# Optimization experiments

Hardware: AMD Instinct MI355X
Metric: run time of the kernel (lower is better)

## Reference

```python
import jax, jax.numpy as jnp
import numpy as np

N_NODES = 100000
N_EDGES = 1600000
IN_DIM, HID, OUT_DIM = 64, 128, 9


def _lin_params(key, fan_in, fan_out, bias=True):
    k1, k2 = jax.random.split(key)
    bound = 1.0 / np.sqrt(fan_in)
    W = jax.random.uniform(k1, (fan_in, fan_out), jnp.float32, -bound, bound)
    if bias:
        b = jax.random.uniform(k2, (fan_out,), jnp.float32, -bound, bound)
        return W, b
    return W


def setup_inputs() -> dict:
    key = jax.random.key(0)
    ks = jax.random.split(key, 12)
    x = jax.random.normal(ks[0], (N_NODES, IN_DIM), jnp.float32)
    edge_index = jax.random.randint(ks[1], (2, N_EDGES), 0, N_NODES, jnp.int64 if jax.config.jax_enable_x64 else jnp.int32)
    Wl1, bl1 = _lin_params(ks[2], IN_DIM, HID)
    Wr1 = _lin_params(ks[3], IN_DIM, HID, bias=False)
    Wl2, bl2 = _lin_params(ks[4], HID, HID)
    Wr2 = _lin_params(ks[5], HID, HID, bias=False)
    Wl3, bl3 = _lin_params(ks[6], HID, 2 * HID)
    Wr3 = _lin_params(ks[7], HID, 2 * HID, bias=False)
    Wfc, bfc = _lin_params(ks[8], 2 * HID, OUT_DIM)
    return {"x": x, "edge_index": edge_index,
            "Wl1": Wl1, "bl1": bl1, "Wr1": Wr1,
            "Wl2": Wl2, "bl2": bl2, "Wr2": Wr2,
            "Wl3": Wl3, "bl3": bl3, "Wr3": Wr3,
            "Wfc": Wfc, "bfc": bfc}


def _sage_conv(x, src, dst, Wl, bl, Wr):
    # PyG SAGEConv (mean aggr): out = lin_l(mean_{j->i} x_j) + lin_r(x_i)
    n = x.shape[0]
    summed = jax.ops.segment_sum(x[src], dst, num_segments=n)         # [N, d]
    deg = jax.ops.segment_sum(jnp.ones((src.shape[0],), x.dtype), dst, num_segments=n)
    mean = summed / jnp.maximum(deg, 1.0)[:, None]
    return mean @ Wl + bl + x @ Wr


def reference(x, edge_index, Wl1, bl1, Wr1, Wl2, bl2, Wr2, Wl3, bl3, Wr3, Wfc, bfc):
    src, dst = edge_index[0], edge_index[1]
    h = jax.nn.relu(_sage_conv(x, src, dst, Wl1, bl1, Wr1))
    h = jax.nn.relu(_sage_conv(h, src, dst, Wl2, bl2, Wr2))
    h = jax.nn.relu(_sage_conv(h, src, dst, Wl3, bl3, Wr3))
    return h @ Wfc + bfc
```

## Files before the change

kernel.cpp:

```cpp
#include <hip/hip_runtime.h>
#include <cstddef>
#include <cstdint>


typedef unsigned int uint_t;
typedef unsigned short ushort_t;
typedef __attribute__((ext_vector_type(8))) short short8;
typedef __attribute__((ext_vector_type(4))) float f32x4;

#define N_IN 64
#define N_HID 128
#define N_OUT 9
#define EB 512
#define NBUCK_MAX 800

__device__ __forceinline__ ushort_t f2bf(float f) {
    uint_t u = __float_as_uint(f);
    u += 0x7fffu + ((u >> 16) & 1u);
    return (ushort_t)(u >> 16);
}
__device__ __forceinline__ float bf2f(ushort_t h) {
    return __uint_as_float(((uint_t)h) << 16);
}
__device__ __forceinline__ void async_ld16(const void* g, void* l) {
    __builtin_amdgcn_global_load_lds((const __attribute__((address_space(1))) void*)g,
                                     (__attribute__((address_space(3))) void*)l, 16, 0, 0);
}

__global__ __launch_bounds__(256) void csr_count(const int* __restrict__ dst,
                                                 uint_t* __restrict__ cnt,
                                                 int E, int nbuck, int chunk) {
    __shared__ uint_t c[NBUCK_MAX];
    for (int i = threadIdx.x; i < nbuck; i += 256) c[i] = 0;
    __syncthreads();
    const int beg = blockIdx.x * chunk;
    const int end = min(beg + chunk, E);
    for (int i = beg + threadIdx.x; i < end; i += 256)
        atomicAdd(&c[dst[i] >> 7], 1u);
    __syncthreads();
    for (int i = threadIdx.x; i < nbuck; i += 256)
        cnt[(size_t)blockIdx.x * nbuck + i] = c[i];
}

__global__ __launch_bounds__(512) void csr_colscan(uint_t* __restrict__ cnt,
                                                   uint_t* __restrict__ total, int nbuck) {
    __shared__ uint_t sm[512];
    const int b = blockIdx.x;
    const uint_t v = cnt[(size_t)threadIdx.x * nbuck + b];
    sm[threadIdx.x] = v;
    __syncthreads();
    for (int off = 1; off < 512; off <<= 1) {
        uint_t t = (threadIdx.x >= off) ? sm[threadIdx.x - off] : 0;
        __syncthreads();
        sm[threadIdx.x] += t;
        __syncthreads();
    }
    cnt[(size_t)threadIdx.x * nbuck + b] = sm[threadIdx.x] - v;
    if (threadIdx.x == 511) total[b] = sm[511];
}

__global__ __launch_bounds__(1024) void top_scan_1024(const uint_t* __restrict__ total,
                                                      uint_t* __restrict__ basev, int nb) {
    __shared__ uint_t sm[1024];
    const int i = threadIdx.x;
    const uint_t v = (i < nb) ? total[i] : 0;
    sm[i] = v;
    __syncthreads();
    for (int off = 1; off < 1024; off <<= 1) {
        uint_t t = (i >= off) ? sm[i - off] : 0;
        __syncthreads();
        sm[i] += t;
        __syncthreads();
    }
    if (i < nb) basev[i] = sm[i] - v;
}

__global__ __launch_bounds__(256) void csr_scatter(const int* __restrict__ src,
                                                   const int* __restrict__ dst,
                                                   const uint_t* __restrict__ cnt,
                                                   const uint_t* __restrict__ basev,
                                                   uint_t* __restrict__ ebuf,
                                                   int E, int nbuck, int chunk) {
    __shared__ uint_t cur[NBUCK_MAX];
    for (int i = threadIdx.x; i < nbuck; i += 256)
        cur[i] = basev[i] + cnt[(size_t)blockIdx.x * nbuck + i];
    __syncthreads();
    const int beg = blockIdx.x * chunk;
    const int end = min(beg + chunk, E);
    for (int i = beg + threadIdx.x; i < end; i += 256) {
        const int d = dst[i];
        const uint_t pos = atomicAdd(&cur[d >> 7], 1u);
        ebuf[pos] = ((uint_t)src[i] << 7) | (uint_t)(d & 127);
    }
}

__global__ __launch_bounds__(256) void csr_final(const uint_t* __restrict__ ebuf,
                                                 const uint_t* __restrict__ basev,
                                                 const uint_t* __restrict__ total,
                                                 int* __restrict__ colA,
                                                 int* __restrict__ row_start,
                                                 int* __restrict__ degi,
                                                 float* __restrict__ invdeg, int M) {
    __shared__ uint_t c128[128];
    __shared__ uint_t cur[128];
    __shared__ uint_t sm[256];
    const int b = blockIdx.x;
    const int nbase = b << 7;
    const uint_t e0 = basev[b];
    const uint_t T = total[b];
    if (threadIdx.x < 128) c128[threadIdx.x] = 0;
    __syncthreads();
    for (uint_t i = threadIdx.x; i < T; i += 256)
        atomicAdd(&c128[ebuf[e0 + i] & 127], 1u);
    __syncthreads();
    const uint_t v = (threadIdx.x < 128) ? c128[threadIdx.x] : 0;
    sm[threadIdx.x] = v;
    __syncthreads();
    for (int off = 1; off < 128; off <<= 1) {
        uint_t t = (threadIdx.x >= off) ? sm[threadIdx.x - off] : 0;
        __syncthreads();
        sm[threadIdx.x] += t;
        __syncthreads();
    }
    if (threadIdx.x < 128) {
        const uint_t ex = sm[threadIdx.x] - v;
        cur[threadIdx.x] = ex;
        const int node = nbase + threadIdx.x;
        if (node < M) {
            degi[node] = (int)v;
            invdeg[node] = 1.0f / fmaxf((float)v, 1.0f);
            row_start[node] = (int)(e0 + ex);
        }
    }
    __syncthreads();
    for (uint_t i = threadIdx.x; i < T; i += 256) {
        const uint_t p = ebuf[e0 + i];
        const uint_t pos = atomicAdd(&cur[p & 127], 1u);
        colA[e0 + pos] = (int)(p >> 7);
    }
}

__global__ void split_x_kernel(const float* __restrict__ X, ushort_t* __restrict__ xh,
                               ushort_t* __restrict__ xl, ushort_t* __restrict__ xrow, int M) {
    int idx = blockIdx.x * 256 + threadIdx.x;
    if (idx >= M * 8) return;
    const int node = idx >> 3;
    const int ch = idx & 7;
    const float4 f0 = *(const float4*)(X + (size_t)node * 64 + ch * 8);
    const float4 f1 = *(const float4*)(X + (size_t)node * 64 + ch * 8 + 4);
    float e[8] = {f0.x, f0.y, f0.z, f0.w, f1.x, f1.y, f1.z, f1.w};
    uint_t hv[4], lv[4];
#pragma unroll
    for (int t = 0; t < 4; ++t) {
        ushort_t h0 = f2bf(e[2 * t]), h1 = f2bf(e[2 * t + 1]);
        ushort_t l0 = f2bf(e[2 * t] - bf2f(h0)), l1 = f2bf(e[2 * t + 1] - bf2f(h1));
        hv[t] = (uint_t)h0 | ((uint_t)h1 << 16);
        lv[t] = (uint_t)l0 | ((uint_t)l1 << 16);
    }
    const size_t off = ((size_t)(node >> 7) * 8 + ch) * 1024 + (node & 127) * 8;
    const uint4 hq = make_uint4(hv[0], hv[1], hv[2], hv[3]);
    *(uint4*)(xh + off) = hq;
    *(uint4*)(xl + off) = make_uint4(lv[0], lv[1], lv[2], lv[3]);
    *(uint4*)(xrow + (size_t)node * 64 + ch * 8) = hq;
}

__global__ __launch_bounds__(256) void wsplit_all(
    const float* __restrict__ Wl1, const float* __restrict__ Wr1,
    const float* __restrict__ Wl2, const float* __restrict__ Wr2,
    const float* __restrict__ Wl3, const float* __restrict__ Wr3,
    ushort_t* __restrict__ w1lh, ushort_t* __restrict__ w1ll,
    ushort_t* __restrict__ w1rh, ushort_t* __restrict__ w1rl,
    ushort_t* __restrict__ w2lh, ushort_t* __restrict__ w2ll,
    ushort_t* __restrict__ w2rh, ushort_t* __restrict__ w2rl,
    ushort_t* __restrict__ w3lh, ushort_t* __restrict__ w3ll,
    ushort_t* __restrict__ w3rh, ushort_t* __restrict__ w3rl)
{
    int idx = blockIdx.x * 256 + threadIdx.x;
    const float* W; ushort_t* th; ushort_t* tl; int K, N, e;
    if (idx < 8192)        { W = Wl1; th = w1lh; tl = w1ll; K = 64;  N = 128; e = idx; }
    else if (idx < 16384)  { W = Wr1; th = w1rh; tl = w1rl; K = 64;  N = 128; e = idx - 8192; }
    else if (idx < 32768)  { W = Wl2; th = w2lh; tl = w2ll; K = 128; N = 128; e = idx - 16384; }
    else if (idx < 49152)  { W = Wr2; th = w2rh; tl = w2rl; K = 128; N = 128; e = idx - 32768; }
    else if (idx < 81920)  { W = Wl3; th = w3lh; tl = w3ll; K = 128; N = 256; e = idx - 49152; }
    else if (idx < 114688) { W = Wr3; th = w3rh; tl = w3rl; K = 128; N = 256; e = idx - 81920; }
    else return;
    int k = e / N, n = e - k * N;
    float v = W[e];
    ushort_t hb = f2bf(v);
    const size_t off = ((size_t)(n >> 7) * (K >> 3) + (k >> 3)) * 1024 + (n & 127) * 8 + (k & 7);
    th[off] = hb;
    tl[off] = f2bf(v - bf2f(hb));
}

__device__ __forceinline__ void acc8_hi(float* a, uint4 h) {
    a[0] += __uint_as_float(h.x << 16);
    a[1] += __uint_as_float(h.x & 0xffff0000u);
    a[2] += __uint_as_float(h.y << 16);
    a[3] += __uint_as_float(h.y & 0xffff0000u);
    a[4] += __uint_as_float(h.z << 16);
    a[5] += __uint_as_float(h.z & 0xffff0000u);
    a[6] += __uint_as_float(h.w << 16);
    a[7] += __uint_as_float(h.w & 0xffff0000u);
}

template <int CH>
__global__ __launch_bounds__(256) void gather_mean_hi(
    const ushort_t* __restrict__ fh, const int* __restrict__ colA,
    const int* __restrict__ row_start, const int* __restrict__ degi,
    const float* __restrict__ invdeg,
    ushort_t* __restrict__ oh, int M)
{
    constexpr int SLOTS = 256 / CH;
    constexpr int DIM = CH * 8;
    const int tid = threadIdx.x;
    const int slot = tid / CH;
    const int ch = tid % CH;
    const int node = blockIdx.x * SLOTS + slot;
    if (node >= M) return;
    const int beg = row_start[node];
    const int cnt = degi[node];
    float a[8];
#pragma unroll
    for (int t = 0; t < 8; ++t) a[t] = 0.f;
    int j = 0;
    for (; j + 3 < cnt; j += 4) {
        const int s0 = colA[beg + j];
        const int s1 = colA[beg + j + 1];
        const int s2 = colA[beg + j + 2];
        const int s3 = colA[beg + j + 3];
        const uint4 h0 = *(const uint4*)(fh + (size_t)s0 * DIM + ch * 8);
        const uint4 h1 = *(const uint4*)(fh + (size_t)s1 * DIM + ch * 8);
        const uint4 h2 = *(const uint4*)(fh + (size_t)s2 * DIM + ch * 8);
        const uint4 h3 = *(const uint4*)(fh + (size_t)s3 * DIM + ch * 8);
        acc8_hi(a, h0);
        acc8_hi(a, h1);
        acc8_hi(a, h2);
        acc8_hi(a, h3);
    }
    for (; j < cnt; ++j) {
        const int s0 = colA[beg + j];
        const uint4 h0 = *(const uint4*)(fh + (size_t)s0 * DIM + ch * 8);
        acc8_hi(a, h0);
    }
    const float sc = invdeg[node];
    uint_t hv[4];
#pragma unroll
    for (int t = 0; t < 4; ++t) {
        ushort_t hb0 = f2bf(a[2 * t] * sc), hb1 = f2bf(a[2 * t + 1] * sc);
        hv[t] = (uint_t)hb0 | ((uint_t)hb1 << 16);
    }
    const size_t off = ((size_t)(node >> 7) * CH + ch) * 1024 + (node & 127) * 8;
    *(uint4*)(oh + off) = make_uint4(hv[0], hv[1], hv[2], hv[3]);
}

__global__ __launch_bounds__(256) void mfma_sage_gemm(
    const ushort_t* __restrict__ Amh,
    const ushort_t* __restrict__ Axh, const ushort_t* __restrict__ Axl,
    const ushort_t* __restrict__ Blh, const ushort_t* __restrict__ Bll,
    const ushort_t* __restrict__ Brh, const ushort_t* __restrict__ Brl,
    const float* __restrict__ bias, ushort_t* __restrict__ Oh,
    ushort_t* __restrict__ Orow,
    int M, int K, int N, int axl_valid)
{
    __shared__ ushort_t As_h[4096];
    __shared__ ushort_t As_l[4096];
    __shared__ ushort_t Bs_h[4096];
    __shared__ ushort_t Bs_l[4096];

    const int tid  = threadIdx.x;
    const int lane = tid & 63;
    const int wave = tid >> 6;
    const int wm = (wave & 1) * 64;
    const int wn = (wave >> 1) * 64;
    const int l15 = lane & 15;
    const int quad = lane >> 4;
    const int bm = blockIdx.x * 128;
    const int bn = blockIdx.y * 128;
    const int KC = K >> 3;

    const int s0 = wave * 1024 + lane * 8;
    const int s1 = s0 + 512;
    const size_t gA_w = ((size_t)blockIdx.x * KC + wave) << 10;
    const size_t gB_w = ((size_t)blockIdx.y * KC + wave) << 10;
    const int l8 = lane * 8;

    f32x4 acc[4][4];
#pragma unroll
    for (int i = 0; i < 4; ++i)
#pragma unroll
        for (int j = 0; j < 4; ++j) acc[i][j] = (f32x4){0.f, 0.f, 0.f, 0.f};

    for (int phase = 0; phase < 2; ++phase) {
        const ushort_t* __restrict__ Ah = phase ? Axh : Amh;
        const ushort_t* __restrict__ Al = phase ? Axl : (const ushort_t*)nullptr;
        const ushort_t* __restrict__ Bh = phase ? Brh : Blh;
        const ushort_t* __restrict__ Bl = phase ? Brl : Bll;
        const bool doAl = (phase == 1) && (axl_valid != 0);
        for (int k0 = 0; k0 < K; k0 += 32) {
            const size_t ga = gA_w + ((size_t)(k0 >> 3) << 10) + l8;
            const size_t gb = gB_w + ((size_t)(k0 >> 3) << 10) + l8;
            __syncthreads();
            async_ld16(Ah + ga, &As_h[s0]);
            async_ld16(Ah + ga + 512, &As_h[s1]);
            if (doAl) {
                async_ld16(Al + ga, &As_l[s0]);
                async_ld16(Al + ga + 512, &As_l[s1]);
            }
            async_ld16(Bh + gb, &Bs_h[s0]);
            async_ld16(Bh + gb + 512, &Bs_h[s1]);
            async_ld16(Bl + gb, &Bs_l[s0]);
            async_ld16(Bl + gb + 512, &Bs_l[s1]);
            __syncthreads();

            short8 fah[4], fal[4], fbh[4], fbl[4];
#pragma unroll
            for (int i = 0; i < 4; ++i) {
                const int aoff = quad * 1024 + (wm + i * 16 + l15) * 8;
                const int boff = quad * 1024 + (wn + i * 16 + l15) * 8;
                fah[i] = *(const short8*)&As_h[aoff];
                fbh[i] = *(const short8*)&Bs_h[boff];
                fbl[i] = *(const short8*)&Bs_l[boff];
                if (doAl) fal[i] = *(const short8*)&As_l[aoff];
            }
#pragma unroll
            for (int i = 0; i < 4; ++i)
#pragma unroll
                for (int j = 0; j < 4; ++j) {
                    acc[i][j] = __builtin_amdgcn_mfma_f32_16x16x32_bf16(fah[i], fbh[j], acc[i][j], 0, 0, 0);
                    acc[i][j] = __builtin_amdgcn_mfma_f32_16x16x32_bf16(fah[i], fbl[j], acc[i][j], 0, 0, 0);
                    if (doAl)
                        acc[i][j] = __builtin_amdgcn_mfma_f32_16x16x32_bf16(fal[i], fbh[j], acc[i][j], 0, 0, 0);
                }
        }
    }

    const size_t otile = (size_t)blockIdx.x * (N >> 3) * 1024;
#pragma unroll
    for (int i = 0; i < 4; ++i) {
        const int mr0 = wm + i * 16 + quad * 4;
#pragma unroll
        for (int j = 0; j < 4; ++j) {
            const int col = bn + wn + j * 16 + l15;
            const float bv = bias[col];
            const size_t cbase = otile + (size_t)(col >> 3) * 1024 + (col & 7);
#pragma unroll
            for (int r = 0; r < 4; ++r) {
                const int row = bm + mr0 + r;
                if (row < M) {
                    float y = fmaxf(acc[i][j][r] + bv, 0.f);
                    const ushort_t hb = f2bf(y);
                    Oh[cbase + (size_t)(mr0 + r) * 8] = hb;
                    if (Orow) Orow[(size_t)row * N + col] = hb;
                }
            }
        }
    }
}

__global__ __launch_bounds__(256) void fc_hi_kernel(
    const ushort_t* __restrict__ hh, const float* __restrict__ W,
    const float* __restrict__ b, float* __restrict__ outp, int M)
{
    __shared__ float Ws[256 * N_OUT];
    __shared__ float bs[N_OUT];
    for (int i = threadIdx.x; i < 256 * N_OUT; i += 256) Ws[i] = W[i];
    if (threadIdx.x < N_OUT) bs[threadIdx.x] = b[threadIdx.x];
    __syncthreads();
    const int t = blockIdx.x * 256 + threadIdx.x;
    if (t >= M * N_OUT) return;
    const int i = t / N_OUT;
    const int j = t - i * N_OUT;
    const ushort_t* __restrict__ base = hh + (size_t)(i >> 7) * 32 * 1024 + (i & 127) * 8;
    float s = bs[j];
#pragma unroll 4
    for (int c = 0; c < 32; ++c) {
        const uint4 v = *(const uint4*)(base + (size_t)c * 1024);
        const uint_t u[4] = {v.x, v.y, v.z, v.w};
#pragma unroll
        for (int q = 0; q < 4; ++q) {
            float a0 = __uint_as_float(u[q] << 16);
            float a1 = __uint_as_float(u[q] & 0xffff0000u);
            s += a0 * Ws[(c * 8 + 2 * q) * N_OUT + j] + a1 * Ws[(c * 8 + 2 * q + 1) * N_OUT + j];
        }
    }
    outp[t] = s;
}

extern "C" void kernel_launch(void* const* d_in, const int* in_sizes, int n_in,
                              void* d_out, int out_size, void* d_ws, size_t ws_size,
                              hipStream_t stream) {
    const float* x   = (const float*)d_in[0];
    const int*   ei  = (const int*)d_in[1];
    const float* Wl1 = (const float*)d_in[2];
    const float* bl1 = (const float*)d_in[3];
    const float* Wr1 = (const float*)d_in[4];
    const float* Wl2 = (const float*)d_in[5];
    const float* bl2 = (const float*)d_in[6];
    const float* Wr2 = (const float*)d_in[7];
    const float* Wl3 = (const float*)d_in[8];
    const float* bl3 = (const float*)d_in[9];
    const float* Wr3 = (const float*)d_in[10];
    const float* Wfc = (const float*)d_in[11];
    const float* bfc = (const float*)d_in[12];
    float* outp = (float*)d_out;

    const int M = in_sizes[0] / N_IN;
    const int E = in_sizes[1] / 2;
    const int* src = ei;
    const int* dst = ei + E;
    const size_t Mrow = 100352;
    const int nbuck = (M + 127) / 128;
    const int chunk = (E + EB - 1) / EB;

    char* base = (char*)d_ws;
    char* p = base;
    int*   degi      = (int*)p;   p += Mrow * 4;
    int*   row_start = (int*)p;   p += Mrow * 4;
    float* invdeg    = (float*)p; p += Mrow * 4;
    uint_t* cnt      = (uint_t*)p; p += (size_t)EB * NBUCK_MAX * 4;
    uint_t* totalv   = (uint_t*)p; p += NBUCK_MAX * 4;
    uint_t* basev    = (uint_t*)p; p += NBUCK_MAX * 4;
    uint_t* ebuf     = (uint_t*)p; p += ((size_t)E + 3) / 4 * 16;
    int*   colA      = (int*)p;   p += ((size_t)E + 3) / 4 * 16;
    ushort_t* xh     = (ushort_t*)p; p += Mrow * 64 * 2;
    ushort_t* xl     = (ushort_t*)p; p += Mrow * 64 * 2;
    ushort_t* xrow   = (ushort_t*)p; p += Mrow * 64 * 2;
    ushort_t* h1h    = (ushort_t*)p; p += Mrow * 128 * 2;
    ushort_t* h1row  = (ushort_t*)p; p += Mrow * 128 * 2;
    size_t r0_used = (size_t)(p - base);
    size_t h3_need = Mrow * 256 * 2;
    ushort_t* h3h = (ushort_t*)base;
    p = base + (r0_used > h3_need ? r0_used : h3_need);
    ushort_t* aggh  = (ushort_t*)p; p += Mrow * 128 * 2;
    ushort_t* h2h   = (ushort_t*)p; p += Mrow * 128 * 2;
    ushort_t* h2row = (ushort_t*)p; p += Mrow * 128 * 2;
    ushort_t* w1lh = (ushort_t*)p; p += 64 * 128 * 2;
    ushort_t* w1ll = (ushort_t*)p; p += 64 * 128 * 2;
    ushort_t* w1rh = (ushort_t*)p; p += 64 * 128 * 2;
    ushort_t* w1rl = (ushort_t*)p; p += 64 * 128 * 2;
    ushort_t* w2lh = (ushort_t*)p; p += 128 * 128 * 2;
    ushort_t* w2ll = (ushort_t*)p; p += 128 * 128 * 2;
    ushort_t* w2rh = (ushort_t*)p; p += 128 * 128 * 2;
    ushort_t* w2rl = (ushort_t*)p; p += 128 * 128 * 2;
    ushort_t* w3lh = (ushort_t*)p; p += 128 * 256 * 2;
    ushort_t* w3ll = (ushort_t*)p; p += 128 * 256 * 2;
    ushort_t* w3rh = (ushort_t*)p; p += 128 * 256 * 2;
    ushort_t* w3rl = (ushort_t*)p; p += 128 * 256 * 2;
    (void)ws_size; (void)n_in; (void)out_size;

    const int blk = 256;
    const int grid_m = (M + 127) / 128;

    csr_count<<<EB, blk, 0, stream>>>(dst, cnt, E, nbuck, chunk);
    csr_colscan<<<nbuck, 512, 0, stream>>>(cnt, totalv, nbuck);
    top_scan_1024<<<1, 1024, 0, stream>>>(totalv, basev, nbuck);
    csr_scatter<<<EB, blk, 0, stream>>>(src, dst, cnt, basev, ebuf, E, nbuck, chunk);
    csr_final<<<nbuck, blk, 0, stream>>>(ebuf, basev, totalv, colA, row_start, degi, invdeg, M);

    split_x_kernel<<<((M * 8) + blk - 1) / blk, blk, 0, stream>>>(x, xh, xl, xrow, M);
    wsplit_all<<<448, blk, 0, stream>>>(Wl1, Wr1, Wl2, Wr2, Wl3, Wr3,
        w1lh, w1ll, w1rh, w1rl, w2lh, w2ll, w2rh, w2rl, w3lh, w3ll, w3rh, w3rl);

    gather_mean_hi<8><<<(M + 31) / 32, blk, 0, stream>>>(
        xrow, colA, row_start, degi, invdeg, aggh, M);
    mfma_sage_gemm<<<dim3(grid_m, 1), blk, 0, stream>>>(
        aggh, xh, xl, w1lh, w1ll, w1rh, w1rl, bl1, h1h, h1row, M, 64, 128, 1);

    gather_mean_hi<16><<<(M + 15) / 16, blk, 0, stream>>>(
        h1row, colA, row_start, degi, invdeg, aggh, M);
    mfma_sage_gemm<<<dim3(grid_m, 1), blk, 0, stream>>>(
        aggh, h1h, (const ushort_t*)nullptr, w2lh, w2ll, w2rh, w2rl, bl2, h2h, h2row, M, 128, 128, 0);

    gather_mean_hi<16><<<(M + 15) / 16, blk, 0, stream>>>(
        h2row, colA, row_start, degi, invdeg, aggh, M);
    mfma_sage_gemm<<<dim3(grid_m, 2), blk, 0, stream>>>(
        aggh, h2h, (const ushort_t*)nullptr, w3lh, w3ll, w3rh, w3rl, bl3, h3h, (ushort_t*)nullptr, M, 128, 256, 0);

    fc_hi_kernel<<<(M * N_OUT + blk - 1) / blk, blk, 0, stream>>>(
        h3h, Wfc, bfc, outp, M);
}
```

Baseline: 463.2 us.

## Fuse final FC into layer-3 GEMM epilogue, merge prep kernels, unroll gather by 8

```diff
diff --git a/kernel.cpp b/kernel.cpp
--- a/kernel.cpp
+++ b/kernel.cpp
@@ -140,31 +140,9 @@
     }
 }
 
-__global__ void split_x_kernel(const float* __restrict__ X, ushort_t* __restrict__ xh,
-                               ushort_t* __restrict__ xl, ushort_t* __restrict__ xrow, int M) {
-    int idx = blockIdx.x * 256 + threadIdx.x;
-    if (idx >= M * 8) return;
-    const int node = idx >> 3;
-    const int ch = idx & 7;
-    const float4 f0 = *(const float4*)(X + (size_t)node * 64 + ch * 8);
-    const float4 f1 = *(const float4*)(X + (size_t)node * 64 + ch * 8 + 4);
-    float e[8] = {f0.x, f0.y, f0.z, f0.w, f1.x, f1.y, f1.z, f1.w};
-    uint_t hv[4], lv[4];
-#pragma unroll
-    for (int t = 0; t < 4; ++t) {
-        ushort_t h0 = f2bf(e[2 * t]), h1 = f2bf(e[2 * t + 1]);
-        ushort_t l0 = f2bf(e[2 * t] - bf2f(h0)), l1 = f2bf(e[2 * t + 1] - bf2f(h1));
-        hv[t] = (uint_t)h0 | ((uint_t)h1 << 16);
-        lv[t] = (uint_t)l0 | ((uint_t)l1 << 16);
-    }
-    const size_t off = ((size_t)(node >> 7) * 8 + ch) * 1024 + (node & 127) * 8;
-    const uint4 hq = make_uint4(hv[0], hv[1], hv[2], hv[3]);
-    *(uint4*)(xh + off) = hq;
-    *(uint4*)(xl + off) = make_uint4(lv[0], lv[1], lv[2], lv[3]);
-    *(uint4*)(xrow + (size_t)node * 64 + ch * 8) = hq;
-}
-
-__global__ __launch_bounds__(256) void wsplit_all(
+__global__ __launch_bounds__(256) void prep_split(
+    const float* __restrict__ X, ushort_t* __restrict__ xh,
+    ushort_t* __restrict__ xl, ushort_t* __restrict__ xrow, int M,
     const float* __restrict__ Wl1, const float* __restrict__ Wr1,
     const float* __restrict__ Wl2, const float* __restrict__ Wr2,
     const float* __restrict__ Wl3, const float* __restrict__ Wr3,
@@ -176,6 +154,29 @@
     ushort_t* __restrict__ w3rh, ushort_t* __restrict__ w3rl)
 {
     int idx = blockIdx.x * 256 + threadIdx.x;
+    const int xn = M * 8;
+    if (idx < xn) {
+        const int node = idx >> 3;
+        const int ch = idx & 7;
+        const float4 f0 = *(const float4*)(X + (size_t)node * 64 + ch * 8);
+        const float4 f1 = *(const float4*)(X + (size_t)node * 64 + ch * 8 + 4);
+        float e[8] = {f0.x, f0.y, f0.z, f0.w, f1.x, f1.y, f1.z, f1.w};
+        uint_t hv[4], lv[4];
+#pragma unroll
+        for (int t = 0; t < 4; ++t) {
+            ushort_t h0 = f2bf(e[2 * t]), h1 = f2bf(e[2 * t + 1]);
+            ushort_t l0 = f2bf(e[2 * t] - bf2f(h0)), l1 = f2bf(e[2 * t + 1] - bf2f(h1));
+            hv[t] = (uint_t)h0 | ((uint_t)h1 << 16);
+            lv[t] = (uint_t)l0 | ((uint_t)l1 << 16);
+        }
+        const size_t off = ((size_t)(node >> 7) * 8 + ch) * 1024 + (node & 127) * 8;
+        const uint4 hq = make_uint4(hv[0], hv[1], hv[2], hv[3]);
+        *(uint4*)(xh + off) = hq;
+        *(uint4*)(xl + off) = make_uint4(lv[0], lv[1], lv[2], lv[3]);
+        *(uint4*)(xrow + (size_t)node * 64 + ch * 8) = hq;
+        return;
+    }
+    idx -= xn;
     const float* W; ushort_t* th; ushort_t* tl; int K, N, e;
     if (idx < 8192)        { W = Wl1; th = w1lh; tl = w1ll; K = 64;  N = 128; e = idx; }
     else if (idx < 16384)  { W = Wr1; th = w1rh; tl = w1rl; K = 64;  N = 128; e = idx - 8192; }
@@ -223,19 +224,16 @@
 #pragma unroll
     for (int t = 0; t < 8; ++t) a[t] = 0.f;
     int j = 0;
-    for (; j + 3 < cnt; j += 4) {
-        const int s0 = colA[beg + j];
-        const int s1 = colA[beg + j + 1];
-        const int s2 = colA[beg + j + 2];
-        const int s3 = colA[beg + j + 3];
-        const uint4 h0 = *(const uint4*)(fh + (size_t)s0 * DIM + ch * 8);
-        const uint4 h1 = *(const uint4*)(fh + (size_t)s1 * DIM + ch * 8);
-        const uint4 h2 = *(const uint4*)(fh + (size_t)s2 * DIM + ch * 8);
-        const uint4 h3 = *(const uint4*)(fh + (size_t)s3 * DIM + ch * 8);
-        acc8_hi(a, h0);
-        acc8_hi(a, h1);
-        acc8_hi(a, h2);
-        acc8_hi(a, h3);
+    for (; j + 7 < cnt; j += 8) {
+        int s[8];
+#pragma unroll
+        for (int q = 0; q < 8; ++q) s[q] = colA[beg + j + q];
+        uint4 h[8];
+#pragma unroll
+        for (int q = 0; q < 8; ++q)
+            h[q] = *(const uint4*)(fh + (size_t)s[q] * DIM + ch * 8);
+#pragma unroll
+        for (int q = 0; q < 8; ++q) acc8_hi(a, h[q]);
     }
     for (; j < cnt; ++j) {
         const int s0 = colA[beg + j];
@@ -253,6 +251,8 @@
     *(uint4*)(oh + off) = make_uint4(hv[0], hv[1], hv[2], hv[3]);
 }
 
+#define YT_STRIDE 134
+template <int DO_FC>
 __global__ __launch_bounds__(256) void mfma_sage_gemm(
     const ushort_t* __restrict__ Amh,
     const ushort_t* __restrict__ Axh, const ushort_t* __restrict__ Axl,
@@ -260,12 +260,15 @@
     const ushort_t* __restrict__ Brh, const ushort_t* __restrict__ Brl,
     const float* __restrict__ bias, ushort_t* __restrict__ Oh,
     ushort_t* __restrict__ Orow,
+    const float* __restrict__ Wfc, float* __restrict__ part,
     int M, int K, int N, int axl_valid)
 {
-    __shared__ ushort_t As_h[4096];
-    __shared__ ushort_t As_l[4096];
-    __shared__ ushort_t Bs_h[4096];
-    __shared__ ushort_t Bs_l[4096];
+    __shared__ ushort_t smem[DO_FC ? (128 * YT_STRIDE) : 16384];
+    __shared__ float wlds[DO_FC ? 1152 : 1];
+    ushort_t* As_h = smem;
+    ushort_t* As_l = smem + 4096;
+    ushort_t* Bs_h = smem + 8192;
+    ushort_t* Bs_l = smem + 12288;
 
     const int tid  = threadIdx.x;
     const int lane = tid & 63;
@@ -334,56 +337,81 @@
         }
     }
 
-    const size_t otile = (size_t)blockIdx.x * (N >> 3) * 1024;
-#pragma unroll
-    for (int i = 0; i < 4; ++i) {
-        const int mr0 = wm + i * 16 + quad * 4;
-#pragma unroll
-        for (int j = 0; j < 4; ++j) {
-            const int col = bn + wn + j * 16 + l15;
-            const float bv = bias[col];
-            const size_t cbase = otile + (size_t)(col >> 3) * 1024 + (col & 7);
-#pragma unroll
-            for (int r = 0; r < 4; ++r) {
-                const int row = bm + mr0 + r;
-                if (row < M) {
-                    float y = fmaxf(acc[i][j][r] + bv, 0.f);
-                    const ushort_t hb = f2bf(y);
-                    Oh[cbase + (size_t)(mr0 + r) * 8] = hb;
-                    if (Orow) Orow[(size_t)row * N + col] = hb;
+    if (!DO_FC) {
+        const size_t otile = (size_t)blockIdx.x * (N >> 3) * 1024;
+#pragma unroll
+        for (int i = 0; i < 4; ++i) {
+            const int mr0 = wm + i * 16 + quad * 4;
+#pragma unroll
+            for (int j = 0; j < 4; ++j) {
+                const int col = bn + wn + j * 16 + l15;
+                const float bv = bias[col];
+                const size_t cbase = otile + (size_t)(col >> 3) * 1024 + (col & 7);
+#pragma unroll
+                for (int r = 0; r < 4; ++r) {
+                    const int row = bm + mr0 + r;
+                    if (row < M) {
+                        float y = fmaxf(acc[i][j][r] + bv, 0.f);
+                        const ushort_t hb = f2bf(y);
+                        Oh[cbase + (size_t)(mr0 + r) * 8] = hb;
+                        if (Orow) Orow[(size_t)row * N + col] = hb;
+                    }
                 }
             }
         }
-    }
-}
-
-__global__ __launch_bounds__(256) void fc_hi_kernel(
-    const ushort_t* __restrict__ hh, const float* __restrict__ W,
-    const float* __restrict__ b, float* __restrict__ outp, int M)
+    } else {
+        __syncthreads();
+        for (int i = tid; i < 1152; i += 256)
+            wlds[i] = Wfc[(size_t)blockIdx.y * 1152 + i];
+#pragma unroll
+        for (int i = 0; i < 4; ++i) {
+            const int mr0 = wm + i * 16 + quad * 4;
+#pragma unroll
+            for (int j = 0; j < 4; ++j) {
+                const int colL = wn + j * 16 + l15;
+                const float bv = bias[bn + colL];
+#pragma unroll
+                for (int r = 0; r < 4; ++r) {
+                    float y = fmaxf(acc[i][j][r] + bv, 0.f);
+                    smem[(mr0 + r) * YT_STRIDE + colL] = f2bf(y);
+                }
+            }
+        }
+        __syncthreads();
+        const int rowL = tid >> 1;
+        const int kh = (tid & 1) * 64;
+        float s[9];
+#pragma unroll
+        for (int fc = 0; fc < 9; ++fc) s[fc] = 0.f;
+        for (int k = 0; k < 64; ++k) {
+            const float y = bf2f(smem[rowL * YT_STRIDE + kh + k]);
+            const float* wr = &wlds[(kh + k) * 9];
+#pragma unroll
+            for (int fc = 0; fc < 9; ++fc) s[fc] += y * wr[fc];
+        }
+#pragma unroll
+        for (int fc = 0; fc < 9; ++fc) s[fc] += __shfl_down(s[fc], 1);
+        const int grow = bm + rowL;
+        if (((tid & 1) == 0) && grow < M) {
+            float* po = part + (size_t)blockIdx.y * (size_t)M * 9 + (size_t)grow * 9;
+#pragma unroll
+            for (int fc = 0; fc < 9; ++fc) po[fc] = s[fc];
+        }
+    }
+}
+
+__global__ __launch_bounds__(256) void fc_sum_kernel(
+    const float* __restrict__ part, const float* __restrict__ b,
+    float* __restrict__ outp, int M)
 {
-    __shared__ float Ws[256 * N_OUT];
     __shared__ float bs[N_OUT];
-    for (int i = threadIdx.x; i < 256 * N_OUT; i += 256) Ws[i] = W[i];
     if (threadIdx.x < N_OUT) bs[threadIdx.x] = b[threadIdx.x];
     __syncthreads();
     const int t = blockIdx.x * 256 + threadIdx.x;
-    if (t >= M * N_OUT) return;
-    const int i = t / N_OUT;
-    const int j = t - i * N_OUT;
-    const ushort_t* __restrict__ base = hh + (size_t)(i >> 7) * 32 * 1024 + (i & 127) * 8;
-    float s = bs[j];
-#pragma unroll 4
-    for (int c = 0; c < 32; ++c) {
-        const uint4 v = *(const uint4*)(base + (size_t)c * 1024);
-        const uint_t u[4] = {v.x, v.y, v.z, v.w};
-#pragma unroll
-        for (int q = 0; q < 4; ++q) {
-            float a0 = __uint_as_float(u[q] << 16);
-            float a1 = __uint_as_float(u[q] & 0xffff0000u);
-            s += a0 * Ws[(c * 8 + 2 * q) * N_OUT + j] + a1 * Ws[(c * 8 + 2 * q + 1) * N_OUT + j];
-        }
-    }
-    outp[t] = s;
+    const int total = M * N_OUT;
+    if (t >= total) return;
+    const int fc = t % N_OUT;
+    outp[t] = part[t] + part[(size_t)M * 9 + t] + bs[fc];
 }
 
 extern "C" void kernel_launch(void* const* d_in, const int* in_sizes, int n_in,
@@ -427,13 +455,10 @@
     ushort_t* xrow   = (ushort_t*)p; p += Mrow * 64 * 2;
     ushort_t* h1h    = (ushort_t*)p; p += Mrow * 128 * 2;
     ushort_t* h1row  = (ushort_t*)p; p += Mrow * 128 * 2;
-    size_t r0_used = (size_t)(p - base);
-    size_t h3_need = Mrow * 256 * 2;
-    ushort_t* h3h = (ushort_t*)base;
-    p = base + (r0_used > h3_need ? r0_used : h3_need);
-    ushort_t* aggh  = (ushort_t*)p; p += Mrow * 128 * 2;
-    ushort_t* h2h   = (ushort_t*)p; p += Mrow * 128 * 2;
-    ushort_t* h2row = (ushort_t*)p; p += Mrow * 128 * 2;
+    ushort_t* aggh   = (ushort_t*)p; p += Mrow * 128 * 2;
+    ushort_t* h2h    = (ushort_t*)p; p += Mrow * 128 * 2;
+    ushort_t* h2row  = (ushort_t*)p; p += Mrow * 128 * 2;
+    float* part      = (float*)p; p += (size_t)2 * M * 9 * 4;
     ushort_t* w1lh = (ushort_t*)p; p += 64 * 128 * 2;
     ushort_t* w1ll = (ushort_t*)p; p += 64 * 128 * 2;
     ushort_t* w1rh = (ushort_t*)p; p += 64 * 128 * 2;
@@ -457,25 +482,30 @@
     csr_scatter<<<EB, blk, 0, stream>>>(src, dst, cnt, basev, ebuf, E, nbuck, chunk);
     csr_final<<<nbuck, blk, 0, stream>>>(ebuf, basev, totalv, colA, row_start, degi, invdeg, M);
 
-    split_x_kernel<<<((M * 8) + blk - 1) / blk, blk, 0, stream>>>(x, xh, xl, xrow, M);
-    wsplit_all<<<448, blk, 0, stream>>>(Wl1, Wr1, Wl2, Wr2, Wl3, Wr3,
-        w1lh, w1ll, w1rh, w1rl, w2lh, w2ll, w2rh, w2rl, w3lh, w3ll, w3rh, w3rl);
+    {
+        const int total = M * 8 + 114688;
+        prep_split<<<(total + blk - 1) / blk, blk, 0, stream>>>(
+            x, xh, xl, xrow, M, Wl1, Wr1, Wl2, Wr2, Wl3, Wr3,
+            w1lh, w1ll, w1rh, w1rl, w2lh, w2ll, w2rh, w2rl, w3lh, w3ll, w3rh, w3rl);
+    }
 
     gather_mean_hi<8><<<(M + 31) / 32, blk, 0, stream>>>(
         xrow, colA, row_start, degi, invdeg, aggh, M);
-    mfma_sage_gemm<<<dim3(grid_m, 1), blk, 0, stream>>>(
-        aggh, xh, xl, w1lh, w1ll, w1rh, w1rl, bl1, h1h, h1row, M, 64, 128, 1);
+    mfma_sage_gemm<0><<<dim3(grid_m, 1), blk, 0, stream>>>(
+        aggh, xh, xl, w1lh, w1ll, w1rh, w1rl, bl1, h1h, h1row,
+        (const float*)nullptr, (float*)nullptr, M, 64, 128, 1);
 
     gather_mean_hi<16><<<(M + 15) / 16, blk, 0, stream>>>(
         h1row, colA, row_start, degi, invdeg, aggh, M);
-    mfma_sage_gemm<<<dim3(grid_m, 1), blk, 0, stream>>>(
-        aggh, h1h, (const ushort_t*)nullptr, w2lh, w2ll, w2rh, w2rl, bl2, h2h, h2row, M, 128, 128, 0);
+    mfma_sage_gemm<0><<<dim3(grid_m, 1), blk, 0, stream>>>(
+        aggh, h1h, (const ushort_t*)nullptr, w2lh, w2ll, w2rh, w2rl, bl2, h2h, h2row,
+        (const float*)nullptr, (float*)nullptr, M, 128, 128, 0);
 
     gather_mean_hi<16><<<(M + 15) / 16, blk, 0, stream>>>(
         h2row, colA, row_start, degi, invdeg, aggh, M);
-    mfma_sage_gemm<<<dim3(grid_m, 2), blk, 0, stream>>>(
-        aggh, h2h, (const ushort_t*)nullptr, w3lh, w3ll, w3rh, w3rl, bl3, h3h, (ushort_t*)nullptr, M, 128, 256, 0);
-
-    fc_hi_kernel<<<(M * N_OUT + blk - 1) / blk, blk, 0, stream>>>(
-        h3h, Wfc, bfc, outp, M);
-}
+    mfma_sage_gemm<1><<<dim3(grid_m, 2), blk, 0, stream>>>(
+        aggh, h2h, (const ushort_t*)nullptr, w3lh, w3ll, w3rh, w3rl, bl3,
+        (ushort_t*)nullptr, (ushort_t*)nullptr, Wfc, part, M, 128, 256, 0);
+
+    fc_sum_kernel<<<(M * N_OUT + blk - 1) / blk, blk, 0, stream>>>(part, bfc, outp, M);
+}
```

Result: no change. 462.3 us (-0.2%).
